# Kernel tuning notes

Hardware: AMD Instinct MI355X
Metric: run time of the kernel (lower is better)

Reference implementation:

```python
import jax, jax.numpy as jnp
import numpy as np

B, L, D = 2, 2048, 1024
H, K = 16, 16
HD = D // H


def setup_inputs() -> dict:
    key = jax.random.key(0)
    k1, k2, k3, k4, k5 = jax.random.split(key, 5)
    x = jax.random.normal(k1, (B, L, D), dtype=jnp.float32)
    # Linear weight (out_features, in_features), small init to keep logits sane
    w_in = jax.random.normal(k2, (3 * D, D), dtype=jnp.float32) * 0.02
    # TISA radial-basis kernel parameters, per (head, kernel)
    kernel_offsets = jax.random.normal(k3, (H, K), dtype=jnp.float32) * 20.0
    kernel_amplitudes = 0.1 + 0.01 * jax.random.normal(k4, (H, K), dtype=jnp.float32)
    kernel_sharpness = 0.1 + 0.01 * jax.random.normal(k5, (H, K), dtype=jnp.float32)
    return {"x": x, "w_in": w_in, "kernel_offsets": kernel_offsets,
            "kernel_amplitudes": kernel_amplitudes, "kernel_sharpness": kernel_sharpness}


def tisa_bias(offsets, amplitudes, sharpness, seq_len):
    # relative positions -(L-1) .. (L-1)  -> per-head RBF positional scores
    rel = jnp.arange(-(seq_len - 1), seq_len, dtype=jnp.float32)  # (2L-1,)
    # scores[h, m] = sum_k amp[h,k] * exp(-|sharp[h,k]| * (off[h,k] - rel[m])^2)
    diff = offsets[:, :, None] - rel[None, None, :]               # (H, K, 2L-1)
    scores = jnp.sum(amplitudes[:, :, None] * jnp.exp(-jnp.abs(sharpness)[:, :, None] * diff * diff), axis=1)  # (H, 2L-1)
    # Toeplitz expansion: bias[h, i, j] = scores[h, (i - j) + (L-1)]
    i = jnp.arange(seq_len)
    idx = i[:, None] - i[None, :] + (seq_len - 1)                 # (L, L)
    return scores[:, idx]                                         # (H, L, L)


def reference(x, w_in, kernel_offsets, kernel_amplitudes, kernel_sharpness):
    b, l, d = x.shape
    proj = jnp.einsum('bld,ed->ble', x, w_in)                     # (B, L, 3D)
    # split: memory = first 2D (k then v), query = last D
    k_, v_, q_ = proj[..., :d], proj[..., d:2 * d], proj[..., 2 * d:]

    def heads(t):
        return t.reshape(b, l, H, HD).transpose(0, 2, 1, 3)       # (B, H, L, HD)

    q, k, v = heads(q_), heads(k_), heads(v_)
    bias = tisa_bias(kernel_offsets, kernel_amplitudes, kernel_sharpness, l)  # (H, L, L)
    scale = 1.0 / np.sqrt(HD).astype(np.float32)
    logits = jnp.einsum('bhld,bhmd->bhlm', q, k) * scale + bias[None]
    attn = jax.nn.softmax(logits, axis=-1)
    out = jnp.einsum('bhlm,bhmd->bhld', attn, v)                  # (B, H, L, HD)
    return out.transpose(0, 2, 1, 3).reshape(b, l, d)             # (B, L, D)
```

## Files before the change

### kernel.cpp

```cpp
#include <hip/hip_runtime.h>
#include <hip/hip_bf16.h>
#include <stdint.h>
#include <stddef.h>


#define NB     2
#define NH     16
#define SL     2048
#define DH     64
#define DMODEL 1024
#define SCP    4096
#define LOG2E  1.44269504088896340736f

typedef __attribute__((ext_vector_type(8)))  short bf16x8;
typedef __attribute__((ext_vector_type(4)))  short bf16x4;
typedef __attribute__((ext_vector_type(4)))  float f32x4;
typedef __attribute__((ext_vector_type(16))) float f32x16;

static __device__ __forceinline__ short f2bf(float x) {
  __hip_bfloat16 h = __float2bfloat16(x);
  return *reinterpret_cast<short*>(&h);
}
static __device__ __forceinline__ short f2bf_fast(float x) {
  union { float f; uint32_t u; } v; v.f = x;
  return (short)((v.u + 0x8000u) >> 16);
}
static __device__ __forceinline__ float fexp2(float x) {
#if __has_builtin(__builtin_amdgcn_exp2f)
  return __builtin_amdgcn_exp2f(x);
#else
  return __expf(x * 0.69314718056f);
#endif
}
static __device__ __forceinline__ uint32_t cvtpk_bf16(float lo, float hi) {
  uint32_t r;
  asm("v_cvt_pk_bf16_f32 %0, %1, %2" : "=v"(r) : "v"(lo), "v"(hi));
  return r;
}
#define PLSWAP(a, b) asm("v_permlane32_swap_b32 %0, %1" : "+v"(a), "+v"(b))

#define GLD(g, l) __builtin_amdgcn_global_load_lds( \
    (const __attribute__((address_space(1))) void*)(g), \
    (__attribute__((address_space(3))) void*)(l), 16, 0, 0)

__global__ __launch_bounds__(256) void prep_k(
    const float* __restrict__ x, const float* __restrict__ w,
    const float* __restrict__ koff, const float* __restrict__ kamp,
    const float* __restrict__ kshp,
    short* __restrict__ xbf, short* __restrict__ wbf,
    float* __restrict__ scores) {
  const int bx = blockIdx.x, tid = threadIdx.x;
  if (bx < 3584) {
    const float* src = (bx < 2048) ? x : w;
    short* dst       = (bx < 2048) ? xbf : wbf;
    const size_t i   = ((size_t)(bx < 2048 ? bx : bx - 2048) * 256 + tid) * 8;
    float4 a = *(const float4*)(src + i);
    float4 b = *(const float4*)(src + i + 4);
    bf16x8 o;
    o[0] = f2bf(a.x); o[1] = f2bf(a.y); o[2] = f2bf(a.z); o[3] = f2bf(a.w);
    o[4] = f2bf(b.x); o[5] = f2bf(b.y); o[6] = f2bf(b.z); o[7] = f2bf(b.w);
    *(bf16x8*)(dst + i) = o;
  } else {
    const int idx = bx - 3584;
    const int h = idx >> 4;
    const int r = (idx & 15) * 256 + tid;
    if (r >= 4095) return;
    float rel = (float)(r - (SL - 1));
    float acc = 0.f;
#pragma unroll
    for (int k = 0; k < 16; ++k) {
      float o = koff[h * 16 + k];
      float a = kamp[h * 16 + k];
      float s = fabsf(kshp[h * 16 + k]);
      float d = o - rel;
      acc += a * __expf(-s * d * d);
    }
    scores[h * SCP + r] = acc * LOG2E;
  }
}

__global__ __launch_bounds__(256) void qkv_gemm_k(
    const short* __restrict__ A, const short* __restrict__ Bw,
    __hip_bfloat16* __restrict__ kbuf, __hip_bfloat16* __restrict__ vbufT,
    __hip_bfloat16* __restrict__ qbuf) {
  __shared__ __align__(16) short SM[12288];
  short* As = SM;
  short* Bs = SM + 8192;
  const int tid  = threadIdx.x;
  const int lane = tid & 63;
  const int wv   = tid >> 6;
  const int l15  = lane & 15, quad = lane >> 4;
  const int wm = (wv & 1) * 64, wn = (wv >> 1) * 32;
  const int xt = blockIdx.x, yt = blockIdx.y;
  const int m0 = yt * 128, n0 = xt * 64;
  const int which = xt >> 4;
  const int hh    = xt & 15;

  f32x4 acc[4][2];
#pragma unroll
  for (int r = 0; r < 4; ++r)
#pragma unroll
    for (int c = 0; c < 2; ++c) acc[r][c] = (f32x4){0.f, 0.f, 0.f, 0.f};

  for (int kt = 0; kt < 16; ++kt) {
    const int k0 = kt * 64;
#pragma unroll
    for (int it = 0; it < 4; ++it) {
      const int e8  = it * 256 + tid;
      GLD(A + (size_t)(m0 + (e8 >> 3)) * DMODEL + k0 + (e8 & 7) * 8, &As[e8 * 8]);
    }
#pragma unroll
    for (int it = 0; it < 2; ++it) {
      const int e8  = it * 256 + tid;
      GLD(Bw + (size_t)(n0 + (e8 >> 3)) * DMODEL + k0 + (e8 & 7) * 8, &Bs[e8 * 8]);
    }
    __syncthreads();
#pragma unroll
    for (int ki = 0; ki < 64; ki += 32) {
      bf16x8 af[4], bfv[2];
#pragma unroll
      for (int r = 0; r < 4; ++r)
        af[r] = *(const bf16x8*)&As[(wm + r * 16 + l15) * 64 + ki + quad * 8];
#pragma unroll
      for (int c = 0; c < 2; ++c)
        bfv[c] = *(const bf16x8*)&Bs[(wn + c * 16 + l15) * 64 + ki + quad * 8];
#pragma unroll
      for (int r = 0; r < 4; ++r)
#pragma unroll
        for (int c = 0; c < 2; ++c)
          acc[r][c] = __builtin_amdgcn_mfma_f32_16x16x32_bf16(af[r], bfv[c], acc[r][c], 0, 0, 0);
    }
    __syncthreads();
  }

  const int bb  = m0 >> 11;
  const int llb = m0 & 2047;
  if (which != 1) {
    const float qs = (which == 2) ? 0.125f * LOG2E : 1.0f;
#pragma unroll
    for (int r = 0; r < 4; ++r)
#pragma unroll
      for (int c = 0; c < 2; ++c)
#pragma unroll
        for (int gg = 0; gg < 4; ++gg)
          SM[(wm + r * 16 + quad * 4 + gg) * 72 + wn + c * 16 + l15] =
              f2bf_fast(acc[r][c][gg] * qs);
    __syncthreads();
    __hip_bfloat16* dst = (which == 0) ? kbuf : qbuf;
#pragma unroll
    for (int i = 0; i < 4; ++i) {
      const int cidx = i * 256 + tid;
      const int m = cidx >> 3, ch = cidx & 7;
      bf16x8 val = *(const bf16x8*)&SM[m * 72 + ch * 8];
      *(bf16x8*)&dst[(((size_t)bb * NH + hh) * SL + llb + m) * DH + ch * 8] = val;
    }
  } else {
#pragma unroll
    for (int r = 0; r < 4; ++r)
#pragma unroll
      for (int c = 0; c < 2; ++c) {
        bf16x4 pk;
#pragma unroll
        for (int gg = 0; gg < 4; ++gg) pk[gg] = f2bf_fast(acc[r][c][gg]);
        *(bf16x4*)&SM[(wn + c * 16 + l15) * 136 + wm + r * 16 + quad * 4] = pk;
      }
    __syncthreads();
#pragma unroll
    for (int i = 0; i < 4; ++i) {
      const int cidx = i * 256 + tid;
      const int n = cidx >> 4, ch = cidx & 15;
      bf16x8 val = *(const bf16x8*)&SM[n * 136 + ch * 8];
      *(bf16x8*)&vbufT[(((size_t)bb * NH + hh) * DH + n) * SL + llb + ch * 8] = val;
    }
  }
}

__global__ __launch_bounds__(512, 4) void attn_k(
    const __hip_bfloat16* __restrict__ qbuf, const __hip_bfloat16* __restrict__ kbuf,
    const __hip_bfloat16* __restrict__ vbufT, const float* __restrict__ scores,
    float* __restrict__ out) {
  __shared__ __align__(16) short Ks[2][64 * 72];
  __shared__ __align__(16) short Vs[2][64 * 72];
  __shared__ __align__(16) float Bt[2][192];
  const int bh   = blockIdx.x;
  const int b    = bh >> 4, h = bh & 15;
  const int tid  = threadIdx.x;
  const int lane = tid & 63;
  const int w    = tid >> 6;
  const int wv   = w & 3;
  const int kw   = w >> 2;
  const int n32  = lane & 31, hf = lane >> 5;
  const int i0b  = blockIdx.y * 128;
  const int i0   = i0b + wv * 32;
  const __hip_bfloat16* qb = qbuf + (size_t)bh * SL * DH;
  const short* kb = (const short*)(kbuf + (size_t)bh * SL * DH);
  const short* vb = (const short*)(vbufT + (size_t)bh * DH * SL);
  const float* sc = scores + h * SCP;

  bf16x8 qf[4];
#pragma unroll
  for (int kc = 0; kc < 4; ++kc)
    qf[kc] = *(const bf16x8*)&qb[(size_t)(i0 + n32) * DH + kc * 16 + hf * 8];

  f32x16 ot[2];
#pragma unroll
  for (int dt = 0; dt < 2; ++dt)
#pragma unroll
    for (int r = 0; r < 16; ++r) ot[dt][r] = 0.f;
  float ls[4] = {0.f, 0.f, 0.f, 0.f};

  auto stage = [&](int bsel, int j0) {
    const short* ksrc = kb + (size_t)j0 * DH;
    {
      int c = tid; int r = c / 9, s = c - r * 9;
      GLD(ksrc + (size_t)r * DH + s * 8, &Ks[bsel][c * 8]);
    }
    if (tid < 64) {
      int c = 512 + tid; int r = c / 9, s = c - r * 9;
      GLD(ksrc + (size_t)r * DH + s * 8, &Ks[bsel][c * 8]);
    }
    {
      int c = tid; int r = c / 9, s = c - r * 9;
      GLD(vb + (size_t)r * SL + j0 + s * 8, &Vs[bsel][c * 8]);
    }
    if (tid < 64) {
      int c = 512 + tid; int r = c / 9, s = c - r * 9;
      GLD(vb + (size_t)r * SL + j0 + s * 8, &Vs[bsel][c * 8]);
    }
    if (tid < 48) GLD(sc + (i0b - j0 + 1984) + tid * 4, &Bt[bsel][tid * 4]);
  };

  auto compute = [&](int bsel) {
    const short* Kp = Ks[bsel];
    const short* Vp = Vs[bsel];
    const float* Bp = Bt[bsel];
    f32x16 st;
    const int tb0 = wv * 32 + n32 - kw * 32 - 4 * hf + 63;
#pragma unroll
    for (int g = 0; g < 4; ++g)
#pragma unroll
      for (int i = 0; i < 4; ++i) st[g * 4 + i] = Bp[tb0 - 8 * g - i];
    __builtin_amdgcn_s_setprio(1);
#pragma unroll
    for (int kc = 0; kc < 4; ++kc) {
      bf16x8 kf = *(const bf16x8*)&Kp[(kw * 32 + n32) * 72 + kc * 16 + hf * 8];
      st = __builtin_amdgcn_mfma_f32_32x32x16_bf16(kf, qf[kc], st, 0, 0, 0);
    }
    __builtin_amdgcn_s_setprio(0);
    float pv[16];
#pragma unroll
    for (int g = 0; g < 4; ++g)
#pragma unroll
      for (int i = 0; i < 4; ++i) {
        pv[g * 4 + i] = fexp2(st[g * 4 + i]);
        ls[g] += pv[g * 4 + i];
      }
    uint32_t a0 = cvtpk_bf16(pv[0],  pv[1]),  a1 = cvtpk_bf16(pv[2],  pv[3]);
    uint32_t b0 = cvtpk_bf16(pv[4],  pv[5]),  b1 = cvtpk_bf16(pv[6],  pv[7]);
    uint32_t c0 = cvtpk_bf16(pv[8],  pv[9]),  c1 = cvtpk_bf16(pv[10], pv[11]);
    uint32_t d0 = cvtpk_bf16(pv[12], pv[13]), d1 = cvtpk_bf16(pv[14], pv[15]);
    PLSWAP(a0, b0); PLSWAP(a1, b1);
    PLSWAP(c0, d0); PLSWAP(c1, d1);
    union { uint32_t u[4]; bf16x8 v; } P0, P1;
    P0.u[0] = a0; P0.u[1] = a1; P0.u[2] = b0; P0.u[3] = b1;
    P1.u[0] = c0; P1.u[1] = c1; P1.u[2] = d0; P1.u[3] = d1;
    const bf16x8 pf0 = P0.v, pf1 = P1.v;
    __builtin_amdgcn_s_setprio(1);
#pragma unroll
    for (int dt = 0; dt < 2; ++dt) {
      const short* vr = &Vp[(dt * 32 + n32) * 72 + kw * 32];
      bf16x8 vf0 = *(const bf16x8*)&vr[hf * 8];
      bf16x8 vf1 = *(const bf16x8*)&vr[16 + hf * 8];
      ot[dt] = __builtin_amdgcn_mfma_f32_32x32x16_bf16(vf0, pf0, ot[dt], 0, 0, 0);
      ot[dt] = __builtin_amdgcn_mfma_f32_32x32x16_bf16(vf1, pf1, ot[dt], 0, 0, 0);
    }
    __builtin_amdgcn_s_setprio(0);
  };

  stage(0, 0);
  __syncthreads();
  int cur = 0;
  for (int j0 = 64; j0 < SL; j0 += 64) {
    stage(cur ^ 1, j0);
    compute(cur);
    __syncthreads();
    cur ^= 1;
  }
  compute(cur);
  __syncthreads();

  float lsum = (ls[0] + ls[1]) + (ls[2] + ls[3]);
  lsum += __shfl_xor(lsum, 32);
  float* red = (wv < 2)
      ? (float*)&Ks[0][0] + ((wv * 64 + lane) * 36)
      : (float*)&Vs[0][0] + (((wv - 2) * 64 + lane) * 36);
  if (kw == 1) {
#pragma unroll
    for (int dt = 0; dt < 2; ++dt)
#pragma unroll
      for (int g = 0; g < 4; ++g) {
        f32x4 v;
#pragma unroll
        for (int i = 0; i < 4; ++i) v[i] = ot[dt][g * 4 + i];
        *(f32x4*)&red[dt * 16 + g * 4] = v;
      }
    red[32] = lsum;
  }
  __syncthreads();
  if (kw == 0) {
#pragma unroll
    for (int dt = 0; dt < 2; ++dt)
#pragma unroll
      for (int g = 0; g < 4; ++g) {
        f32x4 v = *(const f32x4*)&red[dt * 16 + g * 4];
#pragma unroll
        for (int i = 0; i < 4; ++i) ot[dt][g * 4 + i] += v[i];
      }
    lsum += red[32];
    const float inv = 1.f / lsum;
    float* orow = out + (((size_t)b * SL + i0 + n32) * NH + h) * DH;
#pragma unroll
    for (int dt = 0; dt < 2; ++dt)
#pragma unroll
      for (int g = 0; g < 4; ++g) {
        f32x4 v;
#pragma unroll
        for (int i = 0; i < 4; ++i) v[i] = ot[dt][g * 4 + i] * inv;
        *(f32x4*)&orow[dt * 32 + 8 * g + 4 * hf] = v;
      }
  }
}

extern "C" void kernel_launch(void* const* d_in, const int* in_sizes, int n_in,
                              void* d_out, int out_size, void* d_ws, size_t ws_size,
                              hipStream_t stream) {
  const float* x    = (const float*)d_in[0];
  const float* w    = (const float*)d_in[1];
  const float* koff = (const float*)d_in[2];
  const float* kamp = (const float*)d_in[3];
  const float* kshp = (const float*)d_in[4];
  float* out = (float*)d_out;

  const size_t per = (size_t)NB * NH * SL * DH;
  const size_t nx  = (size_t)NB * SL * DMODEL;
  const size_t nw  = (size_t)3 * DMODEL * DMODEL;

  __hip_bfloat16* kbuf  = (__hip_bfloat16*)d_ws;
  __hip_bfloat16* vbufT = kbuf + per;
  __hip_bfloat16* qbuf  = vbufT + per;
  float* scores = (float*)(qbuf + per);
  short* xbf    = (short*)(scores + (size_t)NH * SCP);
  short* wbf    = xbf + nx;

  prep_k<<<3840, 256, 0, stream>>>(x, w, koff, kamp, kshp, xbf, wbf, scores);
  qkv_gemm_k<<<dim3(48, 32), 256, 0, stream>>>(xbf, wbf, kbuf, vbufT, qbuf);
  attn_k<<<dim3(NB * NH, SL / 128), 512, 0, stream>>>(qbuf, kbuf, vbufT, scores, out);
}
```

Baseline: 170.1 us.

## Triple-buffer K/V tiles and prefetch next tile's fragments into registers

Moves the attention inner loop from double to triple buffering of the K, V and bias tiles in shared memory. The loop is unrolled by two with ping-pong register sets, so the K fragments and bias-initialised scores for the next tile are read from LDS while the current tile is computed. This aims to hide LDS read latency and the global-to-LDS load latency behind MFMA work. In exchange it adds about 50% more shared memory and extra live registers, which may lower occupancy under the 512-thread launch bounds.

```diff
diff --git a/kernel.cpp b/kernel.cpp
--- a/kernel.cpp
+++ b/kernel.cpp
@@ -179,9 +179,9 @@
     const __hip_bfloat16* __restrict__ qbuf, const __hip_bfloat16* __restrict__ kbuf,
     const __hip_bfloat16* __restrict__ vbufT, const float* __restrict__ scores,
     float* __restrict__ out) {
-  __shared__ __align__(16) short Ks[2][64 * 72];
-  __shared__ __align__(16) short Vs[2][64 * 72];
-  __shared__ __align__(16) float Bt[2][192];
+  __shared__ __align__(16) short Ks[3][64 * 72];
+  __shared__ __align__(16) short Vs[3][64 * 72];
+  __shared__ __align__(16) float Bt[3][192];
   const int bh   = blockIdx.x;
   const int b    = bh >> 4, h = bh & 15;
   const int tid  = threadIdx.x;
@@ -209,6 +209,9 @@
     for (int r = 0; r < 16; ++r) ot[dt][r] = 0.f;
   float ls[4] = {0.f, 0.f, 0.f, 0.f};
 
+  const int kfoff = (kw * 32 + n32) * 72 + hf * 8;
+  const int tb0   = wv * 32 + n32 - kw * 32 - 4 * hf + 63;
+
   auto stage = [&](int bsel, int j0) {
     const short* ksrc = kb + (size_t)j0 * DH;
     {
@@ -230,35 +233,35 @@
     if (tid < 48) GLD(sc + (i0b - j0 + 1984) + tid * 4, &Bt[bsel][tid * 4]);
   };
 
-  auto compute = [&](int bsel) {
-    const short* Kp = Ks[bsel];
+  auto loadF = [&](bf16x8 (&kf)[4], f32x16& st, int bsel) {
+#pragma unroll
+    for (int kc = 0; kc < 4; ++kc)
+      kf[kc] = *(const bf16x8*)&Ks[bsel][kfoff + kc * 16];
+    const float* Bp = Bt[bsel];
+#pragma unroll
+    for (int g = 0; g < 4; ++g)
+#pragma unroll
+      for (int i = 0; i < 4; ++i) st[g * 4 + i] = Bp[tb0 - 8 * g - i];
+  };
+
+  auto compute = [&](bf16x8 (&kf)[4], f32x16& st, int bsel) {
     const short* Vp = Vs[bsel];
-    const float* Bp = Bt[bsel];
-    f32x16 st;
-    const int tb0 = wv * 32 + n32 - kw * 32 - 4 * hf + 63;
+    __builtin_amdgcn_s_setprio(1);
+#pragma unroll
+    for (int kc = 0; kc < 4; ++kc)
+      st = __builtin_amdgcn_mfma_f32_32x32x16_bf16(kf[kc], qf[kc], st, 0, 0, 0);
+    __builtin_amdgcn_s_setprio(0);
 #pragma unroll
     for (int g = 0; g < 4; ++g)
 #pragma unroll
-      for (int i = 0; i < 4; ++i) st[g * 4 + i] = Bp[tb0 - 8 * g - i];
-    __builtin_amdgcn_s_setprio(1);
-#pragma unroll
-    for (int kc = 0; kc < 4; ++kc) {
-      bf16x8 kf = *(const bf16x8*)&Kp[(kw * 32 + n32) * 72 + kc * 16 + hf * 8];
-      st = __builtin_amdgcn_mfma_f32_32x32x16_bf16(kf, qf[kc], st, 0, 0, 0);
-    }
-    __builtin_amdgcn_s_setprio(0);
-    float pv[16];
-#pragma unroll
-    for (int g = 0; g < 4; ++g)
-#pragma unroll
       for (int i = 0; i < 4; ++i) {
-        pv[g * 4 + i] = fexp2(st[g * 4 + i]);
-        ls[g] += pv[g * 4 + i];
-      }
-    uint32_t a0 = cvtpk_bf16(pv[0],  pv[1]),  a1 = cvtpk_bf16(pv[2],  pv[3]);
-    uint32_t b0 = cvtpk_bf16(pv[4],  pv[5]),  b1 = cvtpk_bf16(pv[6],  pv[7]);
-    uint32_t c0 = cvtpk_bf16(pv[8],  pv[9]),  c1 = cvtpk_bf16(pv[10], pv[11]);
-    uint32_t d0 = cvtpk_bf16(pv[12], pv[13]), d1 = cvtpk_bf16(pv[14], pv[15]);
+        st[g * 4 + i] = fexp2(st[g * 4 + i]);
+        ls[g] += st[g * 4 + i];
+      }
+    uint32_t a0 = cvtpk_bf16(st[0],  st[1]),  a1 = cvtpk_bf16(st[2],  st[3]);
+    uint32_t b0 = cvtpk_bf16(st[4],  st[5]),  b1 = cvtpk_bf16(st[6],  st[7]);
+    uint32_t c0 = cvtpk_bf16(st[8],  st[9]),  c1 = cvtpk_bf16(st[10], st[11]);
+    uint32_t d0 = cvtpk_bf16(st[12], st[13]), d1 = cvtpk_bf16(st[14], st[15]);
     PLSWAP(a0, b0); PLSWAP(a1, b1);
     PLSWAP(c0, d0); PLSWAP(c1, d1);
     union { uint32_t u[4]; bf16x8 v; } P0, P1;
@@ -277,17 +280,26 @@
     __builtin_amdgcn_s_setprio(0);
   };
 
+  bf16x8 kfA[4], kfB[4];
+  f32x16 stA, stB;
   stage(0, 0);
+  stage(1, 64);
   __syncthreads();
-  int cur = 0;
-  for (int j0 = 64; j0 < SL; j0 += 64) {
-    stage(cur ^ 1, j0);
-    compute(cur);
-    __syncthreads();
-    cur ^= 1;
-  }
-  compute(cur);
-  __syncthreads();
+  loadF(kfA, stA, 0);
+  int bcur = 0, bnxt = 1, bfar = 2;
+#pragma unroll 1
+  for (int t = 0; t < 32; t += 2) {
+    if (t + 2 < 32) stage(bfar, (t + 2) * 64);
+    loadF(kfB, stB, bnxt);
+    compute(kfA, stA, bcur);
+    __syncthreads();
+    { int tmp = bcur; bcur = bnxt; bnxt = bfar; bfar = tmp; }
+    if (t + 3 < 32) stage(bfar, (t + 3) * 64);
+    if (t + 2 < 32) loadF(kfA, stA, bnxt);
+    compute(kfB, stB, bcur);
+    __syncthreads();
+    { int tmp = bcur; bcur = bnxt; bnxt = bfar; bfar = tmp; }
+  }
 
   float lsum = (ls[0] + ls[1]) + (ls[2] + ls[3]);
   lsum += __shfl_xor(lsum, 32);
```

Result: slower. 248.0 us (+45.8%).
